# Kernel tuning notes

Measured on AMD Instinct MI355X. Metric: run time of the kernel, lower is better.

## Reference

```python
import jax, jax.numpy as jnp
import numpy as np

V, D, L, H, S = 32000, 512, 4, 8, 2048
HD = D // H
EPS = 1e-5

def setup_inputs() -> dict:
    key = jax.random.key(0)
    ks = jax.random.split(key, 20)
    std = 0.02
    inp = {
        'input_ids': jax.random.randint(ks[0], (2, S), 0, V),
        'tok_emb': jax.random.normal(ks[1], (V, D), jnp.float32) * std,
        'pos_emb': jax.random.normal(ks[2], (S, D), jnp.float32) * std,
        'ln1_w': jnp.ones((L, D), jnp.float32),
        'ln1_b': jnp.zeros((L, D), jnp.float32),
        'qkv_w': jax.random.normal(ks[3], (L, D, 3 * D), jnp.float32) * std,
        'qkv_b': jnp.zeros((L, 3 * D), jnp.float32),
        'proj_w': jax.random.normal(ks[4], (L, D, D), jnp.float32) * std,
        'proj_b': jnp.zeros((L, D), jnp.float32),
        'ln2_w': jnp.ones((L, D), jnp.float32),
        'ln2_b': jnp.zeros((L, D), jnp.float32),
        'fc1_w': jax.random.normal(ks[5], (L, D, 4 * D), jnp.float32) * std,
        'fc1_b': jnp.zeros((L, 4 * D), jnp.float32),
        'fc2_w': jax.random.normal(ks[6], (L, 4 * D, D), jnp.float32) * std,
        'fc2_b': jnp.zeros((L, D), jnp.float32),
        'lnf_w': jnp.ones((D,), jnp.float32),
        'lnf_b': jnp.zeros((D,), jnp.float32),
    }
    return inp

def _layernorm(x, w, b):
    mu = jnp.mean(x, axis=-1, keepdims=True)
    var = jnp.mean(jnp.square(x - mu), axis=-1, keepdims=True)
    return (x - mu) * jax.lax.rsqrt(var + EPS) * w + b

def _attn(x, qkv_w, qkv_b, proj_w, proj_b):
    B, T, C = x.shape
    qkv = x @ qkv_w + qkv_b                       # [B,T,3D]
    q, k, v = jnp.split(qkv, 3, axis=-1)
    q = q.reshape(B, T, H, HD)
    k = k.reshape(B, T, H, HD)
    v = v.reshape(B, T, H, HD)
    att = jnp.einsum('bthd,bshd->bhts', q, k) / jnp.sqrt(jnp.float32(HD))
    causal = jnp.tril(jnp.ones((T, T), bool))
    att = jnp.where(causal, att, -jnp.inf)
    att = jax.nn.softmax(att, axis=-1)
    y = jnp.einsum('bhts,bshd->bthd', att, v).reshape(B, T, C)
    return y @ proj_w + proj_b

def reference(input_ids, tok_emb, pos_emb, ln1_w, ln1_b, qkv_w, qkv_b,
              proj_w, proj_b, ln2_w, ln2_b, fc1_w, fc1_b, fc2_w, fc2_b,
              lnf_w, lnf_b):
    B, T = input_ids.shape
    x = tok_emb[input_ids] + pos_emb[:T]          # [B,T,D]
    for i in range(L):
        h = _layernorm(x, ln1_w[i], ln1_b[i])
        x = x + _attn(h, qkv_w[i], qkv_b[i], proj_w[i], proj_b[i])
        h = _layernorm(x, ln2_w[i], ln2_b[i])
        h = jax.nn.gelu(h @ fc1_w[i] + fc1_b[i], approximate=False)
        x = x + (h @ fc2_w[i] + fc2_b[i])
    x = _layernorm(x, lnf_w, lnf_b)
    return x @ tok_emb.T                          # tied head -> [B,T,V]
```

## Files before the change

### kernel.cpp

```cpp
#include <hip/hip_runtime.h>
#include <math.h>

#define V_SZ 32000
#define D_SZ 512
#define NL 4
#define NH 8
#define SEQ 2048
#define HD 64
#define NB 2
#define M_ROWS (NB * SEQ)

typedef __attribute__((ext_vector_type(8))) short bf16x8;
typedef __attribute__((ext_vector_type(4))) float f32x4;

__device__ __forceinline__ unsigned short f2bf(float f) {
    unsigned int x = __float_as_uint(f);
    unsigned int r = (x + 0x7FFFu + ((x >> 16) & 1u)) >> 16;
    return (unsigned short)r;
}

__device__ __forceinline__ float gelu_f(float x) {
    return 0.5f * x * (1.0f + erff(x * 0.70710678118654752f));
}

__device__ __forceinline__ void gload16(const void* g, void* l) {
    __builtin_amdgcn_global_load_lds(
        (const __attribute__((address_space(1))) void*)g,
        (__attribute__((address_space(3))) void*)l, 16, 0, 0);
}

__global__ __launch_bounds__(256) void embed_kernel(
    const int* __restrict__ ids, const float* __restrict__ tok,
    const float* __restrict__ pos, float* __restrict__ x) {
    int idx = blockIdx.x * 256 + threadIdx.x;
    int row = idx >> 9;
    int d = idx & 511;
    int t = row & (SEQ - 1);
    x[idx] = tok[(size_t)ids[row] * D_SZ + d] + pos[(size_t)t * D_SZ + d];
}

__global__ __launch_bounds__(256) void ln_kernel(
    const float* __restrict__ x, const float* __restrict__ w,
    const float* __restrict__ b, unsigned short* __restrict__ out) {
    int row = blockIdx.x * 4 + (threadIdx.x >> 6);
    int lane = threadIdx.x & 63;
    const float* xr = x + (size_t)row * D_SZ + lane * 8;
    float4 v0 = *(const float4*)xr;
    float4 v1 = *(const float4*)(xr + 4);
    float s = ((v0.x + v0.y) + (v0.z + v0.w)) + ((v1.x + v1.y) + (v1.z + v1.w));
    #pragma unroll
    for (int off = 1; off < 64; off <<= 1) s += __shfl_xor(s, off);
    float mu = s * (1.0f / 512.0f);
    float d0 = v0.x - mu, d1 = v0.y - mu, d2 = v0.z - mu, d3 = v0.w - mu;
    float d4 = v1.x - mu, d5 = v1.y - mu, d6 = v1.z - mu, d7 = v1.w - mu;
    float q = ((d0 * d0 + d1 * d1) + (d2 * d2 + d3 * d3)) +
              ((d4 * d4 + d5 * d5) + (d6 * d6 + d7 * d7));
    #pragma unroll
    for (int off = 1; off < 64; off <<= 1) q += __shfl_xor(q, off);
    float rs = rsqrtf(q * (1.0f / 512.0f) + 1e-5f);
    const float* wp = w + lane * 8;
    const float* bp = b + lane * 8;
    float4 w0 = *(const float4*)wp, w1 = *(const float4*)(wp + 4);
    float4 b0 = *(const float4*)bp, b1 = *(const float4*)(bp + 4);
    uint4 pk;
    pk.x = (unsigned)f2bf(d0 * rs * w0.x + b0.x) | ((unsigned)f2bf(d1 * rs * w0.y + b0.y) << 16);
    pk.y = (unsigned)f2bf(d2 * rs * w0.z + b0.z) | ((unsigned)f2bf(d3 * rs * w0.w + b0.w) << 16);
    pk.z = (unsigned)f2bf(d4 * rs * w1.x + b1.x) | ((unsigned)f2bf(d5 * rs * w1.y + b1.y) << 16);
    pk.w = (unsigned)f2bf(d6 * rs * w1.z + b1.z) | ((unsigned)f2bf(d7 * rs * w1.w + b1.w) << 16);
    *(uint4*)(out + (size_t)row * D_SZ + lane * 8) = pk;
}

__global__ __launch_bounds__(256) void tconv_kernel(
    const float* __restrict__ in, unsigned short* __restrict__ out, int K, int N) {
    __shared__ float t[32][33];
    int l = blockIdx.z;
    in += (size_t)l * K * N;
    out += (size_t)l * N * K;
    int n0 = blockIdx.x * 32, k0 = blockIdx.y * 32;
    int tx = threadIdx.x & 31, ty = threadIdx.x >> 5;
    #pragma unroll
    for (int p = 0; p < 4; p++) {
        int k = ty + p * 8;
        t[k][tx] = in[(size_t)(k0 + k) * N + n0 + tx];
    }
    __syncthreads();
    #pragma unroll
    for (int p = 0; p < 4; p++) {
        int n = ty + p * 8;
        out[(size_t)(n0 + n) * K + k0 + tx] = f2bf(t[tx][n]);
    }
}

__global__ __launch_bounds__(256) void conv_kernel(
    const float* __restrict__ in, unsigned short* __restrict__ out) {
    int i = blockIdx.x * 256 + threadIdx.x;
    float4 v = ((const float4*)in)[i];
    ushort4 u;
    u.x = f2bf(v.x); u.y = f2bf(v.y); u.z = f2bf(v.z); u.w = f2bf(v.w);
    ((ushort4*)out)[i] = u;
}

__global__ __launch_bounds__(256) void mattn_kernel(
    const unsigned short* __restrict__ qkv, unsigned short* __restrict__ att) {
    __shared__ unsigned short Ks[64][72];
    __shared__ unsigned short Vt[64][72];
    __shared__ unsigned short Ps[4][16][72];
    int id = blockIdx.x;
    int bh = id >> 5;
    int jraw = id & 31;
    int jt = (id < 256) ? jraw : (31 - jraw);
    int b = bh >> 3, h = bh & 7;
    int tid = threadIdx.x, lane = tid & 63, wid = tid >> 6;
    int q15 = lane & 15, g = lane >> 4;
    int qglob = jt * 64 + wid * 16 + q15;
    const unsigned short* base = qkv + (size_t)b * SEQ * (3 * D_SZ);
    const unsigned short* qptr = base + (size_t)qglob * (3 * D_SZ) + h * HD;
    bf16x8 qf0 = *(const bf16x8*)(qptr + g * 8);
    bf16x8 qf1 = *(const bf16x8*)(qptr + 32 + g * 8);

    f32x4 OT[4];
    f32x4 zero = {0.0f, 0.0f, 0.0f, 0.0f};
    #pragma unroll
    for (int n = 0; n < 4; n++) OT[n] = zero;
    float mrun = -1e30f, lrun = 0.0f;

    int krow = tid >> 3, kprt = tid & 7;
    const unsigned short* kbase = base + D_SZ + h * HD + kprt * 8;
    const unsigned short* vbase = base + 2 * D_SZ + h * HD + kprt * 8;
    bf16x8 kp0, kp1, vp0, vp1;

    kp0 = *(const bf16x8*)(kbase + (size_t)krow * (3 * D_SZ));
    kp1 = *(const bf16x8*)(kbase + (size_t)(32 + krow) * (3 * D_SZ));
    vp0 = *(const bf16x8*)(vbase + (size_t)(2 * krow) * (3 * D_SZ));
    vp1 = *(const bf16x8*)(vbase + (size_t)(2 * krow + 1) * (3 * D_SZ));

    int nt = jt + 1;
    for (int st = 0; st < nt; st++) {
        int s0 = st * 64;
        __syncthreads();
        *(bf16x8*)&Ks[krow][kprt * 8] = kp0;
        *(bf16x8*)&Ks[32 + krow][kprt * 8] = kp1;
        {
            int col = (((krow >> 2) ^ kprt) << 3) | ((2 * krow) & 7);
            #pragma unroll
            for (int i = 0; i < 8; i++) {
                int d = kprt * 8 + i;
                unsigned w = (unsigned)(unsigned short)vp0[i]
                           | ((unsigned)(unsigned short)vp1[i] << 16);
                *(unsigned*)&Vt[d][col] = w;
            }
        }
        __syncthreads();
        if (st + 1 < nt) {
            int s1 = s0 + 64;
            kp0 = *(const bf16x8*)(kbase + (size_t)(s1 + krow) * (3 * D_SZ));
            kp1 = *(const bf16x8*)(kbase + (size_t)(s1 + 32 + krow) * (3 * D_SZ));
            vp0 = *(const bf16x8*)(vbase + (size_t)(s1 + 2 * krow) * (3 * D_SZ));
            vp1 = *(const bf16x8*)(vbase + (size_t)(s1 + 2 * krow + 1) * (3 * D_SZ));
        }

        f32x4 S[4];
        #pragma unroll
        for (int n = 0; n < 4; n++) S[n] = zero;
        #pragma unroll
        for (int n = 0; n < 4; n++)
            S[n] = __builtin_amdgcn_mfma_f32_16x16x32_bf16(
                *(const bf16x8*)&Ks[n * 16 + q15][g * 8], qf0, S[n], 0, 0, 0);
        #pragma unroll
        for (int n = 0; n < 4; n++)
            S[n] = __builtin_amdgcn_mfma_f32_16x16x32_bf16(
                *(const bf16x8*)&Ks[n * 16 + q15][32 + g * 8], qf1, S[n], 0, 0, 0);

        bool diag = (st == jt);
        float sm[4][4];
        float mloc = -1e30f;
        #pragma unroll
        for (int n = 0; n < 4; n++)
            #pragma unroll
            for (int r = 0; r < 4; r++) {
                float s = S[n][r] * 0.125f;
                if (diag && (s0 + n * 16 + g * 4 + r) > qglob) s = -1e30f;
                sm[n][r] = s;
                mloc = fmaxf(mloc, s);
            }
        mloc = fmaxf(mloc, __shfl_xor(mloc, 16));
        mloc = fmaxf(mloc, __shfl_xor(mloc, 32));
        float mnew = fmaxf(mrun, mloc);
        float corr = __expf(mrun - mnew);
        lrun *= corr;
        #pragma unroll
        for (int n = 0; n < 4; n++) OT[n] *= corr;
        float lsum = 0.0f;
        #pragma unroll
        for (int n = 0; n < 4; n++) {
            float p0 = __expf(sm[n][0] - mnew);
            float p1 = __expf(sm[n][1] - mnew);
            float p2 = __expf(sm[n][2] - mnew);
            float p3 = __expf(sm[n][3] - mnew);
            lsum += (p0 + p1) + (p2 + p3);
            uint2 pk;
            pk.x = (unsigned)f2bf(p0) | ((unsigned)f2bf(p1) << 16);
            pk.y = (unsigned)f2bf(p2) | ((unsigned)f2bf(p3) << 16);
            *(uint2*)&Ps[wid][q15][n * 16 + g * 4] = pk;
        }
        lsum += __shfl_xor(lsum, 16);
        lsum += __shfl_xor(lsum, 32);
        lrun += lsum;
        mrun = mnew;

        #pragma unroll
        for (int ks = 0; ks < 2; ks++) {
            bf16x8 bp = *(const bf16x8*)&Ps[wid][q15][ks * 32 + g * 8];
            #pragma unroll
            for (int n = 0; n < 4; n++) {
                int d = n * 16 + q15;
                int col = (((ks * 4 + g) ^ ((d >> 3) & 7)) << 3);
                OT[n] = __builtin_amdgcn_mfma_f32_16x16x32_bf16(
                    *(const bf16x8*)&Vt[d][col], bp, OT[n], 0, 0, 0);
            }
        }
    }

    float inv = 1.0f / lrun;
    unsigned short* orow = att + ((size_t)(b * SEQ) + qglob) * D_SZ + h * HD;
    #pragma unroll
    for (int n = 0; n < 4; n++) {
        uint2 u;
        u.x = (unsigned)f2bf(OT[n][0] * inv) | ((unsigned)f2bf(OT[n][1] * inv) << 16);
        u.y = (unsigned)f2bf(OT[n][2] * inv) | ((unsigned)f2bf(OT[n][3] * inv) << 16);
        *(uint2*)(orow + n * 16 + g * 4) = u;
    }
}

template <int BM, int BN, int BK, int WC, bool BIAS, bool GELU_, bool RESID,
          bool OUTBF, bool SWAPXY>
__global__ __launch_bounds__(256) void mgemm_kernel(
    const unsigned short* __restrict__ A,
    const unsigned short* __restrict__ Bt,
    const float* __restrict__ bias,
    const float* __restrict__ resid,
    void* __restrict__ Cv, int M, int N, int K) {
    constexpr int WR = 4 / WC;
    constexpr int WRM = BM / WR;
    constexpr int WCN = BN / WC;
    constexpr int FM = WRM / 16;
    constexpr int FN = WCN / 16;
    constexpr int CPR = BK / 8;
    constexpr int LA = BM * CPR / 256;
    constexpr int LB = BN * CPR / 256;
    __shared__ __attribute__((aligned(16))) unsigned short As[2][BM][BK];
    __shared__ __attribute__((aligned(16))) unsigned short Bs[2][BN][BK];
    int tid = threadIdx.x;
    int lane = tid & 63;
    int wid = tid >> 6;
    int wr = wid / WC, wc = wid % WC;
    int m0 = (SWAPXY ? blockIdx.x : blockIdx.y) * BM;
    int n0 = (SWAPXY ? blockIdx.y : blockIdx.x) * BN;
    int r16 = lane & 15, kg = lane >> 4;

    f32x4 acc[FM][FN];
    f32x4 zero = {0.0f, 0.0f, 0.0f, 0.0f};
    #pragma unroll
    for (int m = 0; m < FM; m++)
        #pragma unroll
        for (int n = 0; n < FN; n++) acc[m][n] = zero;

    const unsigned short* Abase = A + (size_t)m0 * K;
    const unsigned short* Bbase = Bt + (size_t)n0 * K;

    #pragma unroll
    for (int i = 0; i < LA; i++) {
        int c = i * 256 + tid;
        gload16(Abase + (size_t)(c / CPR) * K + (c % CPR) * 8,
                &As[0][c / CPR][(c % CPR) * 8]);
    }
    #pragma unroll
    for (int i = 0; i < LB; i++) {
        int c = i * 256 + tid;
        gload16(Bbase + (size_t)(c / CPR) * K + (c % CPR) * 8,
                &Bs[0][c / CPR][(c % CPR) * 8]);
    }
    __syncthreads();

    unsigned short* a_cur = &As[0][0][0];
    unsigned short* a_nxt = &As[1][0][0];
    unsigned short* b_cur = &Bs[0][0][0];
    unsigned short* b_nxt = &Bs[1][0][0];

    for (int k0 = 0; k0 < K; k0 += BK) {
        if (k0 + BK < K) {
            #pragma unroll
            for (int i = 0; i < LA; i++) {
                int c = i * 256 + tid;
                gload16(Abase + (size_t)(c / CPR) * K + (k0 + BK) + (c % CPR) * 8,
                        a_nxt + c * 8);
            }
            #pragma unroll
            for (int i = 0; i < LB; i++) {
                int c = i * 256 + tid;
                gload16(Bbase + (size_t)(c / CPR) * K + (k0 + BK) + (c % CPR) * 8,
                        b_nxt + c * 8);
            }
        }
        #pragma unroll
        for (int kk = 0; kk < BK / 32; kk++) {
            bf16x8 af[FM], bfr[FN];
            #pragma unroll
            for (int m = 0; m < FM; m++)
                af[m] = *(const bf16x8*)&a_cur[(wr * WRM + m * 16 + r16) * BK +
                                               kk * 32 + kg * 8];
            #pragma unroll
            for (int n = 0; n < FN; n++)
                bfr[n] = *(const bf16x8*)&b_cur[(wc * WCN + n * 16 + r16) * BK +
                                                kk * 32 + kg * 8];
            #pragma unroll
            for (int m = 0; m < FM; m++)
                #pragma unroll
                for (int n = 0; n < FN; n++)
                    acc[m][n] = __builtin_amdgcn_mfma_f32_16x16x32_bf16(
                        af[m], bfr[n], acc[m][n], 0, 0, 0);
        }
        __syncthreads();
        unsigned short* t;
        t = a_cur; a_cur = a_nxt; a_nxt = t;
        t = b_cur; b_cur = b_nxt; b_nxt = t;
    }

    #pragma unroll
    for (int n = 0; n < FN; n++) {
        int col = n0 + wc * WCN + n * 16 + r16;
        float bv = BIAS ? bias[col] : 0.0f;
        #pragma unroll
        for (int m = 0; m < FM; m++) {
            int rb = m0 + wr * WRM + m * 16 + kg * 4;
            #pragma unroll
            for (int r = 0; r < 4; r++) {
                float v = acc[m][n][r] + bv;
                if (GELU_) v = gelu_f(v);
                if (RESID) v += resid[(size_t)(rb + r) * N + col];
                if (OUTBF)
                    ((unsigned short*)Cv)[(size_t)(rb + r) * N + col] = f2bf(v);
                else
                    ((float*)Cv)[(size_t)(rb + r) * N + col] = v;
            }
        }
    }
}

extern "C" void kernel_launch(void* const* d_in, const int* in_sizes, int n_in,
                              void* d_out, int out_size, void* d_ws, size_t ws_size,
                              hipStream_t stream) {
    const int*   ids   = (const int*)d_in[0];
    const float* tok   = (const float*)d_in[1];
    const float* pos   = (const float*)d_in[2];
    const float* ln1w  = (const float*)d_in[3];
    const float* ln1b  = (const float*)d_in[4];
    const float* qkvw  = (const float*)d_in[5];
    const float* qkvb  = (const float*)d_in[6];
    const float* projw = (const float*)d_in[7];
    const float* projb = (const float*)d_in[8];
    const float* ln2w  = (const float*)d_in[9];
    const float* ln2b  = (const float*)d_in[10];
    const float* fc1w  = (const float*)d_in[11];
    const float* fc1b  = (const float*)d_in[12];
    const float* fc2w  = (const float*)d_in[13];
    const float* fc2b  = (const float*)d_in[14];
    const float* lnfw  = (const float*)d_in[15];
    const float* lnfb  = (const float*)d_in[16];
    float* out = (float*)d_out;

    float* x = (float*)d_ws;
    unsigned short* hb = (unsigned short*)(x + (size_t)M_ROWS * D_SZ);
    unsigned short* wq = hb + (size_t)M_ROWS * D_SZ;
    unsigned short* wp = wq + (size_t)NL * D_SZ * 3 * D_SZ;
    unsigned short* w1 = wp + (size_t)NL * D_SZ * D_SZ;
    unsigned short* w2 = w1 + (size_t)NL * D_SZ * 4 * D_SZ;
    unsigned short* qkvb_a = w2 + (size_t)NL * 4 * D_SZ * D_SZ;
    unsigned short* attb = qkvb_a + (size_t)M_ROWS * 3 * D_SZ;
    unsigned short* ffnb = attb + (size_t)M_ROWS * D_SZ;
    unsigned short* tokb = qkvb_a;

    tconv_kernel<<<dim3(1536/32, 512/32, NL), 256, 0, stream>>>(qkvw, wq, D_SZ, 3*D_SZ);
    tconv_kernel<<<dim3(512/32, 512/32, NL), 256, 0, stream>>>(projw, wp, D_SZ, D_SZ);
    tconv_kernel<<<dim3(2048/32, 512/32, NL), 256, 0, stream>>>(fc1w, w1, D_SZ, 4*D_SZ);
    tconv_kernel<<<dim3(512/32, 2048/32, NL), 256, 0, stream>>>(fc2w, w2, 4*D_SZ, D_SZ);

    embed_kernel<<<M_ROWS * D_SZ / 256, 256, 0, stream>>>(ids, tok, pos, x);

    for (int l = 0; l < NL; l++) {
        ln_kernel<<<M_ROWS / 4, 256, 0, stream>>>(x, ln1w + l * D_SZ, ln1b + l * D_SZ, hb);
        mgemm_kernel<64, 128, 64, 2, true, false, false, true, false>
            <<<dim3(3 * D_SZ / 128, M_ROWS / 64), 256, 0, stream>>>(
                hb, wq + (size_t)l * 3 * D_SZ * D_SZ, qkvb + (size_t)l * 3 * D_SZ,
                nullptr, qkvb_a, M_ROWS, 3 * D_SZ, D_SZ);
        mattn_kernel<<<(SEQ / 64) * NB * NH, 256, 0, stream>>>(qkvb_a, attb);
        mgemm_kernel<64, 64, 64, 2, true, false, true, false, false>
            <<<dim3(D_SZ / 64, M_ROWS / 64), 256, 0, stream>>>(
                attb, wp + (size_t)l * D_SZ * D_SZ, projb + (size_t)l * D_SZ,
                x, x, M_ROWS, D_SZ, D_SZ);
        ln_kernel<<<M_ROWS / 4, 256, 0, stream>>>(x, ln2w + l * D_SZ, ln2b + l * D_SZ, hb);
        mgemm_kernel<64, 128, 64, 2, true, true, false, true, false>
            <<<dim3(4 * D_SZ / 128, M_ROWS / 64), 256, 0, stream>>>(
                hb, w1 + (size_t)l * 4 * D_SZ * D_SZ, fc1b + (size_t)l * 4 * D_SZ,
                nullptr, ffnb, M_ROWS, 4 * D_SZ, D_SZ);
        mgemm_kernel<64, 64, 64, 2, true, false, true, false, false>
            <<<dim3(D_SZ / 64, M_ROWS / 64), 256, 0, stream>>>(
                ffnb, w2 + (size_t)l * D_SZ * 4 * D_SZ, fc2b + (size_t)l * D_SZ,
                x, x, M_ROWS, D_SZ, 4 * D_SZ);
    }

    ln_kernel<<<M_ROWS / 4, 256, 0, stream>>>(x, lnfw, lnfb, hb);
    conv_kernel<<<V_SZ * D_SZ / 4 / 256, 256, 0, stream>>>(tok, tokb);
    mgemm_kernel<128, 128, 32, 2, false, false, false, false, true>
        <<<dim3(M_ROWS / 128, V_SZ / 128), 256, 0, stream>>>(
            hb, tokb, nullptr, nullptr, out, M_ROWS, V_SZ, D_SZ);
}
```

Measured before the change: 773.5 us.

## Fuse layernorm into QKV/FC1 GEMMs and merge prep/conversion launches

Drops the standalone layernorm kernels before the QKV and FC1 GEMMs. Those GEMMs now compute per-row mean and rstd from the fp32 residual, then normalise and convert the A tile to bf16 while staging it into shared memory. The weight transposes and the embedding become one combined prep launch, and the final layernorm is merged with the token-embedding bf16 conversion, which cuts launch count and the bf16 activation round trip. In exchange, the fused GEMMs re-read fp32 rows per N-tile, lose the async global-to-LDS A loads, and compute variance as E[x²]−mu², which is numerically less stable.

```diff
diff --git a/kernel.cpp b/kernel.cpp
--- a/kernel.cpp
+++ b/kernel.cpp
@@ -29,54 +29,17 @@
         (__attribute__((address_space(3))) void*)l, 16, 0, 0);
 }
 
-__global__ __launch_bounds__(256) void embed_kernel(
-    const int* __restrict__ ids, const float* __restrict__ tok,
-    const float* __restrict__ pos, float* __restrict__ x) {
-    int idx = blockIdx.x * 256 + threadIdx.x;
-    int row = idx >> 9;
-    int d = idx & 511;
-    int t = row & (SEQ - 1);
-    x[idx] = tok[(size_t)ids[row] * D_SZ + d] + pos[(size_t)t * D_SZ + d];
-}
-
-__global__ __launch_bounds__(256) void ln_kernel(
-    const float* __restrict__ x, const float* __restrict__ w,
-    const float* __restrict__ b, unsigned short* __restrict__ out) {
-    int row = blockIdx.x * 4 + (threadIdx.x >> 6);
-    int lane = threadIdx.x & 63;
-    const float* xr = x + (size_t)row * D_SZ + lane * 8;
-    float4 v0 = *(const float4*)xr;
-    float4 v1 = *(const float4*)(xr + 4);
-    float s = ((v0.x + v0.y) + (v0.z + v0.w)) + ((v1.x + v1.y) + (v1.z + v1.w));
-    #pragma unroll
-    for (int off = 1; off < 64; off <<= 1) s += __shfl_xor(s, off);
-    float mu = s * (1.0f / 512.0f);
-    float d0 = v0.x - mu, d1 = v0.y - mu, d2 = v0.z - mu, d3 = v0.w - mu;
-    float d4 = v1.x - mu, d5 = v1.y - mu, d6 = v1.z - mu, d7 = v1.w - mu;
-    float q = ((d0 * d0 + d1 * d1) + (d2 * d2 + d3 * d3)) +
-              ((d4 * d4 + d5 * d5) + (d6 * d6 + d7 * d7));
-    #pragma unroll
-    for (int off = 1; off < 64; off <<= 1) q += __shfl_xor(q, off);
-    float rs = rsqrtf(q * (1.0f / 512.0f) + 1e-5f);
-    const float* wp = w + lane * 8;
-    const float* bp = b + lane * 8;
-    float4 w0 = *(const float4*)wp, w1 = *(const float4*)(wp + 4);
-    float4 b0 = *(const float4*)bp, b1 = *(const float4*)(bp + 4);
-    uint4 pk;
-    pk.x = (unsigned)f2bf(d0 * rs * w0.x + b0.x) | ((unsigned)f2bf(d1 * rs * w0.y + b0.y) << 16);
-    pk.y = (unsigned)f2bf(d2 * rs * w0.z + b0.z) | ((unsigned)f2bf(d3 * rs * w0.w + b0.w) << 16);
-    pk.z = (unsigned)f2bf(d4 * rs * w1.x + b1.x) | ((unsigned)f2bf(d5 * rs * w1.y + b1.y) << 16);
-    pk.w = (unsigned)f2bf(d6 * rs * w1.z + b1.z) | ((unsigned)f2bf(d7 * rs * w1.w + b1.w) << 16);
-    *(uint4*)(out + (size_t)row * D_SZ + lane * 8) = pk;
-}
-
-__global__ __launch_bounds__(256) void tconv_kernel(
-    const float* __restrict__ in, unsigned short* __restrict__ out, int K, int N) {
-    __shared__ float t[32][33];
-    int l = blockIdx.z;
+__device__ __forceinline__ void tconv_body(
+    const float* __restrict__ in, unsigned short* __restrict__ out,
+    int K, int N, int lin, float (*t)[33]) {
+    int nx = N / 32, ny = K / 32;
+    int bx = lin % nx;
+    int r2 = lin / nx;
+    int by = r2 % ny;
+    int l = r2 / ny;
     in += (size_t)l * K * N;
     out += (size_t)l * N * K;
-    int n0 = blockIdx.x * 32, k0 = blockIdx.y * 32;
+    int n0 = bx * 32, k0 = by * 32;
     int tx = threadIdx.x & 31, ty = threadIdx.x >> 5;
     #pragma unroll
     for (int p = 0; p < 4; p++) {
@@ -91,13 +54,76 @@
     }
 }
 
-__global__ __launch_bounds__(256) void conv_kernel(
-    const float* __restrict__ in, unsigned short* __restrict__ out) {
-    int i = blockIdx.x * 256 + threadIdx.x;
-    float4 v = ((const float4*)in)[i];
-    ushort4 u;
-    u.x = f2bf(v.x); u.y = f2bf(v.y); u.z = f2bf(v.z); u.w = f2bf(v.w);
-    ((ushort4*)out)[i] = u;
+#define TCQ 3072
+#define TCP 1024
+#define TC1 4096
+#define TC2 4096
+#define EMB 8192
+
+__global__ __launch_bounds__(256) void prep_kernel(
+    const float* __restrict__ qkvw, const float* __restrict__ projw,
+    const float* __restrict__ fc1w, const float* __restrict__ fc2w,
+    const int* __restrict__ ids, const float* __restrict__ tok,
+    const float* __restrict__ pos,
+    unsigned short* __restrict__ wq, unsigned short* __restrict__ wp,
+    unsigned short* __restrict__ w1, unsigned short* __restrict__ w2,
+    float* __restrict__ x) {
+    __shared__ float t[32][33];
+    int b = blockIdx.x;
+    if (b < TCQ) { tconv_body(qkvw, wq, D_SZ, 3 * D_SZ, b, t); return; }
+    b -= TCQ;
+    if (b < TCP) { tconv_body(projw, wp, D_SZ, D_SZ, b, t); return; }
+    b -= TCP;
+    if (b < TC1) { tconv_body(fc1w, w1, D_SZ, 4 * D_SZ, b, t); return; }
+    b -= TC1;
+    if (b < TC2) { tconv_body(fc2w, w2, 4 * D_SZ, D_SZ, b, t); return; }
+    b -= TC2;
+    int idx = b * 256 + threadIdx.x;
+    int row = idx >> 9;
+    int d = idx & 511;
+    int tt = row & (SEQ - 1);
+    x[idx] = tok[(size_t)ids[row] * D_SZ + d] + pos[(size_t)tt * D_SZ + d];
+}
+
+__global__ __launch_bounds__(256) void lnconv_kernel(
+    const float* __restrict__ x, const float* __restrict__ w,
+    const float* __restrict__ b, unsigned short* __restrict__ out,
+    const float* __restrict__ tok, unsigned short* __restrict__ tokb) {
+    int blk = blockIdx.x;
+    if (blk < M_ROWS / 4) {
+        int row = blk * 4 + (threadIdx.x >> 6);
+        int lane = threadIdx.x & 63;
+        const float* xr = x + (size_t)row * D_SZ + lane * 8;
+        float4 v0 = *(const float4*)xr;
+        float4 v1 = *(const float4*)(xr + 4);
+        float s = ((v0.x + v0.y) + (v0.z + v0.w)) + ((v1.x + v1.y) + (v1.z + v1.w));
+        #pragma unroll
+        for (int off = 1; off < 64; off <<= 1) s += __shfl_xor(s, off);
+        float mu = s * (1.0f / 512.0f);
+        float d0 = v0.x - mu, d1 = v0.y - mu, d2 = v0.z - mu, d3 = v0.w - mu;
+        float d4 = v1.x - mu, d5 = v1.y - mu, d6 = v1.z - mu, d7 = v1.w - mu;
+        float q = ((d0 * d0 + d1 * d1) + (d2 * d2 + d3 * d3)) +
+                  ((d4 * d4 + d5 * d5) + (d6 * d6 + d7 * d7));
+        #pragma unroll
+        for (int off = 1; off < 64; off <<= 1) q += __shfl_xor(q, off);
+        float rs = rsqrtf(q * (1.0f / 512.0f) + 1e-5f);
+        const float* wp = w + lane * 8;
+        const float* bp = b + lane * 8;
+        float4 w0 = *(const float4*)wp, w1 = *(const float4*)(wp + 4);
+        float4 b0 = *(const float4*)bp, b1 = *(const float4*)(bp + 4);
+        uint4 pk;
+        pk.x = (unsigned)f2bf(d0 * rs * w0.x + b0.x) | ((unsigned)f2bf(d1 * rs * w0.y + b0.y) << 16);
+        pk.y = (unsigned)f2bf(d2 * rs * w0.z + b0.z) | ((unsigned)f2bf(d3 * rs * w0.w + b0.w) << 16);
+        pk.z = (unsigned)f2bf(d4 * rs * w1.x + b1.x) | ((unsigned)f2bf(d5 * rs * w1.y + b1.y) << 16);
+        pk.w = (unsigned)f2bf(d6 * rs * w1.z + b1.z) | ((unsigned)f2bf(d7 * rs * w1.w + b1.w) << 16);
+        *(uint4*)(out + (size_t)row * D_SZ + lane * 8) = pk;
+    } else {
+        int i = (blk - M_ROWS / 4) * 256 + threadIdx.x;
+        float4 v = ((const float4*)tok)[i];
+        ushort4 u;
+        u.x = f2bf(v.x); u.y = f2bf(v.y); u.z = f2bf(v.z); u.w = f2bf(v.w);
+        ((ushort4*)tokb)[i] = u;
+    }
 }
 
 __global__ __launch_bounds__(256) void mattn_kernel(
@@ -233,13 +259,14 @@
 }
 
 template <int BM, int BN, int BK, int WC, bool BIAS, bool GELU_, bool RESID,
-          bool OUTBF, bool SWAPXY>
+          bool OUTBF, bool SWAPXY, bool LNF>
 __global__ __launch_bounds__(256) void mgemm_kernel(
     const unsigned short* __restrict__ A,
     const unsigned short* __restrict__ Bt,
     const float* __restrict__ bias,
     const float* __restrict__ resid,
-    void* __restrict__ Cv, int M, int N, int K) {
+    void* __restrict__ Cv, int M, int N, int K,
+    const float* __restrict__ lnw, const float* __restrict__ lnb) {
     constexpr int WR = 4 / WC;
     constexpr int WRM = BM / WR;
     constexpr int WCN = BN / WC;
@@ -248,8 +275,11 @@
     constexpr int CPR = BK / 8;
     constexpr int LA = BM * CPR / 256;
     constexpr int LB = BN * CPR / 256;
+    static_assert(!LNF || (BM == 64 && BK == 64), "LNF assumes BM=64,BK=64");
     __shared__ __attribute__((aligned(16))) unsigned short As[2][BM][BK];
     __shared__ __attribute__((aligned(16))) unsigned short Bs[2][BN][BK];
+    __shared__ float mu_s[LNF ? BM : 1];
+    __shared__ float rs_s[LNF ? BM : 1];
     int tid = threadIdx.x;
     int lane = tid & 63;
     int wid = tid >> 6;
@@ -265,20 +295,77 @@
         #pragma unroll
         for (int n = 0; n < FN; n++) acc[m][n] = zero;
 
+    const float* X = LNF ? (const float*)A : nullptr;
     const unsigned short* Abase = A + (size_t)m0 * K;
     const unsigned short* Bbase = Bt + (size_t)n0 * K;
 
-    #pragma unroll
-    for (int i = 0; i < LA; i++) {
-        int c = i * 256 + tid;
-        gload16(Abase + (size_t)(c / CPR) * K + (c % CPR) * 8,
-                &As[0][c / CPR][(c % CPR) * 8]);
-    }
-    #pragma unroll
-    for (int i = 0; i < LB; i++) {
-        int c = i * 256 + tid;
-        gload16(Bbase + (size_t)(c / CPR) * K + (c % CPR) * 8,
-                &Bs[0][c / CPR][(c % CPR) * 8]);
+    if constexpr (LNF) {
+        int r = tid >> 2, p = tid & 3;
+        const float* xr = X + (size_t)(m0 + r) * 512 + p * 128;
+        float s = 0.f, q = 0.f;
+        #pragma unroll
+        for (int i = 0; i < 32; i++) {
+            float4 v = ((const float4*)xr)[i];
+            s += (v.x + v.y) + (v.z + v.w);
+            q += (v.x * v.x + v.y * v.y) + (v.z * v.z + v.w * v.w);
+        }
+        s += __shfl_xor(s, 1); s += __shfl_xor(s, 2);
+        q += __shfl_xor(q, 1); q += __shfl_xor(q, 2);
+        if (p == 0) {
+            float mu = s * (1.0f / 512.0f);
+            mu_s[r] = mu;
+            rs_s[r] = rsqrtf(q * (1.0f / 512.0f) - mu * mu + 1e-5f);
+        }
+        __syncthreads();
+    }
+
+    auto stageA_ln = [&](int k0, unsigned short* as) {
+        #pragma unroll
+        for (int i = 0; i < LA; i++) {
+            int c = i * 256 + tid;
+            int r = c >> 3, c8 = c & 7;
+            const float* src = X + (size_t)(m0 + r) * 512 + k0 + c8 * 8;
+            float4 v0 = ((const float4*)src)[0];
+            float4 v1 = ((const float4*)src)[1];
+            const float* wp8 = lnw + k0 + c8 * 8;
+            const float* bp8 = lnb + k0 + c8 * 8;
+            float4 w0 = ((const float4*)wp8)[0], w1v = ((const float4*)wp8)[1];
+            float4 b0 = ((const float4*)bp8)[0], b1v = ((const float4*)bp8)[1];
+            float mm = mu_s[r], rr = rs_s[r];
+            uint4 pk;
+            pk.x = (unsigned)f2bf((v0.x - mm) * rr * w0.x + b0.x)
+                 | ((unsigned)f2bf((v0.y - mm) * rr * w0.y + b0.y) << 16);
+            pk.y = (unsigned)f2bf((v0.z - mm) * rr * w0.z + b0.z)
+                 | ((unsigned)f2bf((v0.w - mm) * rr * w0.w + b0.w) << 16);
+            pk.z = (unsigned)f2bf((v1.x - mm) * rr * w1v.x + b1v.x)
+                 | ((unsigned)f2bf((v1.y - mm) * rr * w1v.y + b1v.y) << 16);
+            pk.w = (unsigned)f2bf((v1.z - mm) * rr * w1v.z + b1v.z)
+                 | ((unsigned)f2bf((v1.w - mm) * rr * w1v.w + b1v.w) << 16);
+            *(uint4*)(as + (size_t)r * BK + c8 * 8) = pk;
+        }
+    };
+
+    if constexpr (LNF) {
+        #pragma unroll
+        for (int i = 0; i < LB; i++) {
+            int c = i * 256 + tid;
+            gload16(Bbase + (size_t)(c / CPR) * K + (c % CPR) * 8,
+                    &Bs[0][c / CPR][(c % CPR) * 8]);
+        }
+        stageA_ln(0, &As[0][0][0]);
+    } else {
+        #pragma unroll
+        for (int i = 0; i < LA; i++) {
+            int c = i * 256 + tid;
+            gload16(Abase + (size_t)(c / CPR) * K + (c % CPR) * 8,
+                    &As[0][c / CPR][(c % CPR) * 8]);
+        }
+        #pragma unroll
+        for (int i = 0; i < LB; i++) {
+            int c = i * 256 + tid;
+            gload16(Bbase + (size_t)(c / CPR) * K + (c % CPR) * 8,
+                    &Bs[0][c / CPR][(c % CPR) * 8]);
+        }
     }
     __syncthreads();
 
@@ -290,16 +377,20 @@
     for (int k0 = 0; k0 < K; k0 += BK) {
         if (k0 + BK < K) {
             #pragma unroll
-            for (int i = 0; i < LA; i++) {
-                int c = i * 256 + tid;
-                gload16(Abase + (size_t)(c / CPR) * K + (k0 + BK) + (c % CPR) * 8,
-                        a_nxt + c * 8);
-            }
-            #pragma unroll
             for (int i = 0; i < LB; i++) {
                 int c = i * 256 + tid;
                 gload16(Bbase + (size_t)(c / CPR) * K + (k0 + BK) + (c % CPR) * 8,
                         b_nxt + c * 8);
+            }
+            if constexpr (LNF) {
+                stageA_ln(k0 + BK, a_nxt);
+            } else {
+                #pragma unroll
+                for (int i = 0; i < LA; i++) {
+                    int c = i * 256 + tid;
+                    gload16(Abase + (size_t)(c / CPR) * K + (k0 + BK) + (c % CPR) * 8,
+                            a_nxt + c * 8);
+                }
             }
         }
         #pragma unroll
@@ -378,40 +469,37 @@
     unsigned short* qkvb_a = w2 + (size_t)NL * 4 * D_SZ * D_SZ;
     unsigned short* attb = qkvb_a + (size_t)M_ROWS * 3 * D_SZ;
     unsigned short* ffnb = attb + (size_t)M_ROWS * D_SZ;
-    unsigned short* tokb = qkvb_a;
-
-    tconv_kernel<<<dim3(1536/32, 512/32, NL), 256, 0, stream>>>(qkvw, wq, D_SZ, 3*D_SZ);
-    tconv_kernel<<<dim3(512/32, 512/32, NL), 256, 0, stream>>>(projw, wp, D_SZ, D_SZ);
-    tconv_kernel<<<dim3(2048/32, 512/32, NL), 256, 0, stream>>>(fc1w, w1, D_SZ, 4*D_SZ);
-    tconv_kernel<<<dim3(512/32, 2048/32, NL), 256, 0, stream>>>(fc2w, w2, 4*D_SZ, D_SZ);
-
-    embed_kernel<<<M_ROWS * D_SZ / 256, 256, 0, stream>>>(ids, tok, pos, x);
+    unsigned short* tokb = wq;
+
+    prep_kernel<<<TCQ + TCP + TC1 + TC2 + EMB, 256, 0, stream>>>(
+        qkvw, projw, fc1w, fc2w, ids, tok, pos, wq, wp, w1, w2, x);
 
     for (int l = 0; l < NL; l++) {
-        ln_kernel<<<M_ROWS / 4, 256, 0, stream>>>(x, ln1w + l * D_SZ, ln1b + l * D_SZ, hb);
-        mgemm_kernel<64, 128, 64, 2, true, false, false, true, false>
+        mgemm_kernel<64, 128, 64, 2, true, false, false, true, false, true>
             <<<dim3(3 * D_SZ / 128, M_ROWS / 64), 256, 0, stream>>>(
-                hb, wq + (size_t)l * 3 * D_SZ * D_SZ, qkvb + (size_t)l * 3 * D_SZ,
-                nullptr, qkvb_a, M_ROWS, 3 * D_SZ, D_SZ);
+                (const unsigned short*)x, wq + (size_t)l * 3 * D_SZ * D_SZ,
+                qkvb + (size_t)l * 3 * D_SZ, nullptr, qkvb_a,
+                M_ROWS, 3 * D_SZ, D_SZ, ln1w + l * D_SZ, ln1b + l * D_SZ);
         mattn_kernel<<<(SEQ / 64) * NB * NH, 256, 0, stream>>>(qkvb_a, attb);
-        mgemm_kernel<64, 64, 64, 2, true, false, true, false, false>
+        mgemm_kernel<64, 64, 64, 2, true, false, true, false, false, false>
             <<<dim3(D_SZ / 64, M_ROWS / 64), 256, 0, stream>>>(
                 attb, wp + (size_t)l * D_SZ * D_SZ, projb + (size_t)l * D_SZ,
-                x, x, M_ROWS, D_SZ, D_SZ);
-        ln_kernel<<<M_ROWS / 4, 256, 0, stream>>>(x, ln2w + l * D_SZ, ln2b + l * D_SZ, hb);
-        mgemm_kernel<64, 128, 64, 2, true, true, false, true, false>
+                x, x, M_ROWS, D_SZ, D_SZ, nullptr, nullptr);
+        mgemm_kernel<64, 128, 64, 2, true, true, false, true, false, true>
             <<<dim3(4 * D_SZ / 128, M_ROWS / 64), 256, 0, stream>>>(
-                hb, w1 + (size_t)l * 4 * D_SZ * D_SZ, fc1b + (size_t)l * 4 * D_SZ,
-                nullptr, ffnb, M_ROWS, 4 * D_SZ, D_SZ);
-        mgemm_kernel<64, 64, 64, 2, true, false, true, false, false>
+                (const unsigned short*)x, w1 + (size_t)l * 4 * D_SZ * D_SZ,
+                fc1b + (size_t)l * 4 * D_SZ, nullptr, ffnb,
+                M_ROWS, 4 * D_SZ, D_SZ, ln2w + l * D_SZ, ln2b + l * D_SZ);
+        mgemm_kernel<64, 64, 64, 2, true, false, true, false, false, false>
             <<<dim3(D_SZ / 64, M_ROWS / 64), 256, 0, stream>>>(
                 ffnb, w2 + (size_t)l * D_SZ * 4 * D_SZ, fc2b + (size_t)l * D_SZ,
-                x, x, M_ROWS, D_SZ, 4 * D_SZ);
-    }
-
-    ln_kernel<<<M_ROWS / 4, 256, 0, stream>>>(x, lnfw, lnfb, hb);
-    conv_kernel<<<V_SZ * D_SZ / 4 / 256, 256, 0, stream>>>(tok, tokb);
-    mgemm_kernel<128, 128, 32, 2, false, false, false, false, true>
+                x, x, M_ROWS, D_SZ, 4 * D_SZ, nullptr, nullptr);
+    }
+
+    lnconv_kernel<<<M_ROWS / 4 + V_SZ * D_SZ / 4 / 256, 256, 0, stream>>>(
+        x, lnfw, lnfb, hb, tok, tokb);
+    mgemm_kernel<128, 128, 32, 2, false, false, false, false, true, false>
         <<<dim3(M_ROWS / 128, V_SZ / 128), 256, 0, stream>>>(
-            hb, tokb, nullptr, nullptr, out, M_ROWS, V_SZ, D_SZ);
-}
+            hb, tokb, nullptr, nullptr, out, M_ROWS, V_SZ, D_SZ,
+            nullptr, nullptr);
+}
```

Measured after the change: 907.3 us. 17.3% more time.
